# Performance work log

Hardware: AMD Instinct MI355X
Metric: run time of the kernel (lower is better)

The kernel has to match this reference:

```python
import jax, jax.numpy as jnp
import numpy as np

B, T, C, H = 2, 2048, 1024, 16
D = C // H  # head_dim = 64
CH = C // 2


def _ln(x, g, b, eps=1e-5):
    m = x.mean(-1, keepdims=True)
    v = ((x - m) ** 2).mean(-1, keepdims=True)
    return (x - m) / jnp.sqrt(v + eps) * g + b


def setup_inputs() -> dict:
    key = jax.random.key(0)
    ks = iter(jax.random.split(key, 32))
    w = lambda shp: jax.random.normal(next(ks), shp, dtype=jnp.float32) * 0.02
    inp = {
        'x': jax.random.normal(next(ks), (B, T, C), dtype=jnp.float32),
        'attention_mask': jnp.ones((B, T, T), dtype=jnp.int32),
        # importance_net: Linear(C,C/2), LN(C/2), GELU, Linear(C/2,1), Sigmoid
        'imp_w1': w((C, CH)), 'imp_b1': jnp.zeros((CH,)),
        'imp_g': jnp.ones((CH,)), 'imp_beta': jnp.zeros((CH,)),
        'imp_w2': w((CH, 1)), 'imp_b2': jnp.zeros((1,)),
        # reasoning_net: Linear(C,C), LN(C), GELU, Linear(C,C)
        'rsn_w1': w((C, C)), 'rsn_b1': jnp.zeros((C,)),
        'rsn_g': jnp.ones((C,)), 'rsn_beta': jnp.zeros((C,)),
        'rsn_w2': w((C, C)), 'rsn_b2': jnp.zeros((C,)),
        # attention projections
        'q_w': w((C, C)), 'q_b': jnp.zeros((C,)),
        'k_w': w((C, C)), 'k_b': jnp.zeros((C,)),
        'v_w': w((C, C)), 'v_b': jnp.zeros((C,)),
        'o_w': w((C, C)), 'o_b': jnp.zeros((C,)),
        # temp_net: Linear(C,C/2), LN(C/2), GELU, Linear(C/2,H)
        'tmp_w1': w((C, CH)), 'tmp_b1': jnp.zeros((CH,)),
        'tmp_g': jnp.ones((CH,)), 'tmp_beta': jnp.zeros((CH,)),
        'tmp_w2': w((CH, H)), 'tmp_b2': jnp.zeros((H,)),
        # output LayerNorm
        'norm_g': jnp.ones((C,)), 'norm_b': jnp.zeros((C,)),
    }
    return inp


def reference(x, attention_mask, imp_w1, imp_b1, imp_g, imp_beta, imp_w2, imp_b2,
              rsn_w1, rsn_b1, rsn_g, rsn_beta, rsn_w2, rsn_b2,
              q_w, q_b, k_w, k_b, v_w, v_b, o_w, o_b,
              tmp_w1, tmp_b1, tmp_g, tmp_beta, tmp_w2, tmp_b2,
              norm_g, norm_b):
    Bz, Tz, Cz = x.shape
    # importance gating: [B,T,1]
    h = jax.nn.gelu(_ln(x @ imp_w1 + imp_b1, imp_g, imp_beta), approximate=False)
    importance = jnp.maximum(jax.nn.sigmoid(h @ imp_w2 + imp_b2), 1e-6)
    xi = x * importance
    # reasoning net on gated input
    h = jax.nn.gelu(_ln(xi @ rsn_w1 + rsn_b1, rsn_g, rsn_beta), approximate=False)
    reasoned = h @ rsn_w2 + rsn_b2
    # projections
    q = (reasoned @ q_w + q_b).reshape(Bz, Tz, H, D).transpose(0, 2, 1, 3)
    k = (xi @ k_w + k_b).reshape(Bz, Tz, H, D).transpose(0, 2, 1, 3)
    v = (x @ v_w + v_b).reshape(Bz, Tz, H, D).transpose(0, 2, 1, 3)
    # per-(batch,head) temperature
    ht = jax.nn.gelu(_ln(reasoned.mean(axis=1) @ tmp_w1 + tmp_b1, tmp_g, tmp_beta), approximate=False)
    temp = jax.nn.softplus(ht @ tmp_w2 + tmp_b2) + 0.5  # [B,H]
    # attention with mask and learned temperature before softmax
    scale = 1.0 / jnp.sqrt(jnp.float32(D))
    attn = jnp.einsum('bhqd,bhkd->bhqk', q, k) * scale
    attn = jnp.where(attention_mask[:, None] == 0, -jnp.inf, attn)
    attn = attn * temp[:, :, None, None]
    attn = jax.nn.softmax(attn, axis=-1)
    # dropout is identity in eval mode
    out = jnp.einsum('bhqk,bhkd->bhqd', attn, v)
    out = out.transpose(0, 2, 1, 3).reshape(Bz, Tz, Cz)
    out = out @ o_w + o_b
    return _ln(x + out, norm_g, norm_b)
```

## Files before the change

kernel.cpp:

```cpp
#include <hip/hip_runtime.h>
#include <hip/hip_bf16.h>
#include <math.h>

#define BB 2
#define TT 2048
#define CC 1024
#define HH 16
#define DD 64
#define CHALF 512
#define NN (BB * TT)
#define LOG2E 1.44269504088896340736f

typedef __attribute__((ext_vector_type(8))) short short8;
typedef __attribute__((ext_vector_type(4))) short short4_t;
typedef __attribute__((ext_vector_type(4))) float f32x4;

__device__ __forceinline__ float gelu_exact(float x) {
    return 0.5f * x * (1.0f + erff(x * 0.70710678118654752f));
}

__device__ __forceinline__ short f2bf(float f) {
    __hip_bfloat16 h = __float2bfloat16(f);
    short s;
    __builtin_memcpy(&s, &h, 2);
    return s;
}

__device__ __forceinline__ void async_copy16(const void* g, void* l) {
    __builtin_amdgcn_global_load_lds(
        (const __attribute__((address_space(1))) void*)g,
        (__attribute__((address_space(3))) void*)l, 16, 0, 0);
}

__global__ __launch_bounds__(256) void prep(
    const float* __restrict__ x, __hip_bfloat16* __restrict__ x_bf,
    const int* __restrict__ mask, int* __restrict__ flags,
    const float* w0, const float* w1, const float* w2, const float* w3,
    const float* w4, const float* w5, const float* w6,
    __hip_bfloat16* t0, __hip_bfloat16* t1, __hip_bfloat16* t2,
    __hip_bfloat16* t3, __hip_bfloat16* t4, __hip_bfloat16* t5,
    __hip_bfloat16* t6) {
    __shared__ float T[64][65];
    int blk = blockIdx.x;
    int tid = threadIdx.x;
    if (blk < 2048) {
        int i = (blk * 256 + tid) * 8;
        float4 a = *(const float4*)&x[i];
        float4 b = *(const float4*)&x[i + 4];
        __hip_bfloat16 o[8] = {
            __float2bfloat16(a.x), __float2bfloat16(a.y),
            __float2bfloat16(a.z), __float2bfloat16(a.w),
            __float2bfloat16(b.x), __float2bfloat16(b.y),
            __float2bfloat16(b.z), __float2bfloat16(b.w)};
        *(float4*)&x_bf[i] = *(float4*)o;
    } else if (blk < 4096) {
        int idx = blk - 2048;
        int kt = idx & 31, qt = (idx >> 5) & 31, b = idx >> 10;
        int* red = (int*)T;
        int r = tid >> 2;
        int c0 = (tid & 3) * 16;
        const int* base =
            mask + ((size_t)(b * TT + qt * 64 + r)) * TT + kt * 64 + c0;
        int all = 1;
#pragma unroll
        for (int i = 0; i < 4; ++i) {
            int4 m4 = *(const int4*)(base + i * 4);
            all &= (m4.x != 0) & (m4.y != 0) & (m4.z != 0) & (m4.w != 0);
        }
        red[tid] = all;
        __syncthreads();
#pragma unroll
        for (int o = 128; o > 0; o >>= 1) {
            if (tid < o) red[tid] &= red[tid + o];
            __syncthreads();
        }
        if (tid == 0) flags[(b * 32 + qt) * 32 + kt] = red[0];
    } else {
        int idx = blk - 4096;
        const float* W;
        __hip_bfloat16* Wt;
        int N, n0, k0;
        if (idx < 128) {
            W = w0; Wt = t0; N = 512;
            n0 = (idx & 7) * 64;
            k0 = (idx >> 3) * 64;
        } else {
            idx -= 128;
            int w = idx >> 8;
            int r = idx & 255;
            N = 1024;
            n0 = (r & 15) * 64;
            k0 = (r >> 4) * 64;
            switch (w) {
                case 0: W = w1; Wt = t1; break;
                case 1: W = w2; Wt = t2; break;
                case 2: W = w3; Wt = t3; break;
                case 3: W = w4; Wt = t4; break;
                case 4: W = w5; Wt = t5; break;
                default: W = w6; Wt = t6; break;
            }
        }
        int c = tid & 63, r4 = tid >> 6;
#pragma unroll
        for (int i = 0; i < 16; ++i) {
            int row = i * 4 + r4;
            T[row][c] = W[(size_t)(k0 + row) * N + n0 + c];
        }
        __syncthreads();
#pragma unroll
        for (int i = 0; i < 16; ++i) {
            int row = i * 4 + r4;
            Wt[(size_t)(n0 + row) * CC + k0 + c] = __float2bfloat16(T[c][row]);
        }
    }
}

template <bool BF16OUT>
__global__ __launch_bounds__(256) void gemm_mfma64(
    const short* __restrict__ A, const short* __restrict__ Wt,
    const float* __restrict__ bias, float* __restrict__ Cf,
    __hip_bfloat16* __restrict__ Cb, int M, int N, int K) {
    __shared__ short As[64][32];
    __shared__ short Bs[128][32];
    int tid = threadIdx.x;
    int wave = tid >> 6, lane = tid & 63;
    int m16 = lane & 15, quad = lane >> 4;
    int wm = wave >> 1, wn = wave & 1;
    int row0 = blockIdx.y * 64, col0 = blockIdx.x * 128;
    int lr = lane >> 2;
    int kof = (lane & 3) * 8;

    f32x4 acc[2][4];
#pragma unroll
    for (int i = 0; i < 2; ++i)
#pragma unroll
        for (int j = 0; j < 4; ++j) acc[i][j] = (f32x4){0.f, 0.f, 0.f, 0.f};

    for (int k0 = 0; k0 < K; k0 += 32) {
        async_copy16(A + (size_t)(row0 + wave * 16 + lr) * K + k0 + kof,
                     &As[wave * 16][0]);
#pragma unroll
        for (int j = 0; j < 2; ++j) {
            int rbase = wave * 32 + j * 16;
            async_copy16(Wt + (size_t)(col0 + rbase + lr) * K + k0 + kof,
                         &Bs[rbase][0]);
        }
        __syncthreads();
        short8 af[2], bfr[4];
#pragma unroll
        for (int i = 0; i < 2; ++i)
            af[i] = *(const short8*)&As[wm * 32 + i * 16 + m16][quad * 8];
#pragma unroll
        for (int j = 0; j < 4; ++j)
            bfr[j] = *(const short8*)&Bs[wn * 64 + j * 16 + m16][quad * 8];
#pragma unroll
        for (int i = 0; i < 2; ++i)
#pragma unroll
            for (int j = 0; j < 4; ++j)
                acc[i][j] = __builtin_amdgcn_mfma_f32_16x16x32_bf16(
                    af[i], bfr[j], acc[i][j], 0, 0, 0);
        __syncthreads();
    }
#pragma unroll
    for (int i = 0; i < 2; ++i) {
#pragma unroll
        for (int j = 0; j < 4; ++j) {
            int col = col0 + wn * 64 + j * 16 + m16;
            float bv = bias[col];
#pragma unroll
            for (int rr = 0; rr < 4; ++rr) {
                int row = row0 + wm * 32 + i * 16 + quad * 4 + rr;
                float val = acc[i][j][rr] + bv;
                if (BF16OUT)
                    Cb[(size_t)row * N + col] = __float2bfloat16(val);
                else
                    Cf[(size_t)row * N + col] = val;
            }
        }
    }
}

__global__ __launch_bounds__(256) void gemm_qkv(
    const short* __restrict__ Aq, const short* __restrict__ Ak,
    const short* __restrict__ Av, const short* __restrict__ Wq,
    const short* __restrict__ Wk, const short* __restrict__ Wv,
    const float* __restrict__ bq, const float* __restrict__ bk,
    const float* __restrict__ bv, __hip_bfloat16* __restrict__ Cq,
    __hip_bfloat16* __restrict__ Ck, __hip_bfloat16* __restrict__ Cv,
    const float* __restrict__ tmp) {
    int z = blockIdx.z;
    const short* A = (z == 0) ? Aq : (z == 1) ? Ak : Av;
    const short* Wt = (z == 0) ? Wq : (z == 1) ? Wk : Wv;
    const float* bias = (z == 0) ? bq : (z == 1) ? bk : bv;
    __hip_bfloat16* C = (z == 0) ? Cq : (z == 1) ? Ck : Cv;

    __shared__ short As[128][32];
    __shared__ short Bs[128][32];
    int tid = threadIdx.x;
    int wave = tid >> 6, lane = tid & 63;
    int m16 = lane & 15, quad = lane >> 4;
    int wm = wave >> 1, wn = wave & 1;
    int row0 = blockIdx.y * 128, col0 = blockIdx.x * 128;
    int lr = lane >> 2;
    int kof = (lane & 3) * 8;

    float scale = 1.0f;
    if (z == 0)
        scale = tmp[(row0 >> 11) * HH + (col0 >> 6) + wn] * 0.125f * LOG2E;

    f32x4 acc[4][4];
#pragma unroll
    for (int i = 0; i < 4; ++i)
#pragma unroll
        for (int j = 0; j < 4; ++j) acc[i][j] = (f32x4){0.f, 0.f, 0.f, 0.f};

    for (int k0 = 0; k0 < CC; k0 += 32) {
#pragma unroll
        for (int j = 0; j < 2; ++j) {
            int rbase = wave * 32 + j * 16;
            async_copy16(A + (size_t)(row0 + rbase + lr) * CC + k0 + kof,
                         &As[rbase][0]);
            async_copy16(Wt + (size_t)(col0 + rbase + lr) * CC + k0 + kof,
                         &Bs[rbase][0]);
        }
        __syncthreads();
        short8 af[4], bfr[4];
#pragma unroll
        for (int i = 0; i < 4; ++i)
            af[i] = *(const short8*)&As[wm * 64 + i * 16 + m16][quad * 8];
#pragma unroll
        for (int j = 0; j < 4; ++j)
            bfr[j] = *(const short8*)&Bs[wn * 64 + j * 16 + m16][quad * 8];
#pragma unroll
        for (int i = 0; i < 4; ++i)
#pragma unroll
            for (int j = 0; j < 4; ++j)
                acc[i][j] = __builtin_amdgcn_mfma_f32_16x16x32_bf16(
                    af[i], bfr[j], acc[i][j], 0, 0, 0);
        __syncthreads();
    }
#pragma unroll
    for (int i = 0; i < 4; ++i) {
#pragma unroll
        for (int j = 0; j < 4; ++j) {
            int col = col0 + wn * 64 + j * 16 + m16;
            float bv2 = bias[col];
#pragma unroll
            for (int rr = 0; rr < 4; ++rr) {
                int row = row0 + wm * 64 + i * 16 + quad * 4 + rr;
                C[(size_t)row * CC + col] =
                    __float2bfloat16((acc[i][j][rr] + bv2) * scale);
            }
        }
    }
}

__global__ __launch_bounds__(256) void imp_fused(
    const float* __restrict__ h1, const float* __restrict__ g,
    const float* __restrict__ beta, const float* __restrict__ w2,
    const float* __restrict__ b2, const float* __restrict__ x,
    __hip_bfloat16* __restrict__ xi) {
    int row = blockIdx.x;
    int tid = threadIdx.x;
    const float* hr = h1 + (size_t)row * CHALF;
    float v0 = hr[tid], v1 = hr[tid + 256];
    __shared__ float red[256];
    red[tid] = v0 + v1;
    __syncthreads();
#pragma unroll
    for (int o = 128; o > 0; o >>= 1) {
        if (tid < o) red[tid] += red[tid + o];
        __syncthreads();
    }
    float mean = red[0] * (1.0f / CHALF);
    __syncthreads();
    float d0 = v0 - mean, d1 = v1 - mean;
    red[tid] = d0 * d0 + d1 * d1;
    __syncthreads();
#pragma unroll
    for (int o = 128; o > 0; o >>= 1) {
        if (tid < o) red[tid] += red[tid + o];
        __syncthreads();
    }
    float inv = rsqrtf(red[0] * (1.0f / CHALF) + 1e-5f);
    __syncthreads();
    float ge0 = gelu_exact(d0 * inv * g[tid] + beta[tid]);
    float ge1 = gelu_exact(d1 * inv * g[tid + 256] + beta[tid + 256]);
    red[tid] = ge0 * w2[tid] + ge1 * w2[tid + 256];
    __syncthreads();
#pragma unroll
    for (int o = 128; o > 0; o >>= 1) {
        if (tid < o) red[tid] += red[tid + o];
        __syncthreads();
    }
    float z = red[0] + b2[0];
    float sg = 1.0f / (1.0f + expf(-z));
    float imp = fmaxf(sg, 1e-6f);
#pragma unroll
    for (int i = 0; i < 4; ++i) {
        int c = i * 256 + tid;
        xi[(size_t)row * CC + c] =
            __float2bfloat16(x[(size_t)row * CC + c] * imp);
    }
}

template <int WIDTH>
__global__ __launch_bounds__(256) void ln_gelu_bf16(
    const float* __restrict__ Y, const float* __restrict__ g,
    const float* __restrict__ beta, __hip_bfloat16* __restrict__ O) {
    constexpr int PT = WIDTH / 256;
    int row = blockIdx.x;
    int tid = threadIdx.x;
    const float* yr = Y + (size_t)row * WIDTH;
    float v[PT];
    float s = 0.f;
#pragma unroll
    for (int i = 0; i < PT; ++i) {
        v[i] = yr[i * 256 + tid];
        s += v[i];
    }
    __shared__ float red[256];
    red[tid] = s;
    __syncthreads();
#pragma unroll
    for (int o = 128; o > 0; o >>= 1) {
        if (tid < o) red[tid] += red[tid + o];
        __syncthreads();
    }
    float mean = red[0] * (1.0f / WIDTH);
    __syncthreads();
    s = 0.f;
#pragma unroll
    for (int i = 0; i < PT; ++i) {
        float d = v[i] - mean;
        s += d * d;
    }
    red[tid] = s;
    __syncthreads();
#pragma unroll
    for (int o = 128; o > 0; o >>= 1) {
        if (tid < o) red[tid] += red[tid + o];
        __syncthreads();
    }
    float inv = rsqrtf(red[0] * (1.0f / WIDTH) + 1e-5f);
#pragma unroll
    for (int i = 0; i < PT; ++i) {
        int c = i * 256 + tid;
        O[(size_t)row * WIDTH + c] =
            __float2bfloat16(gelu_exact((v[i] - mean) * inv * g[c] + beta[c]));
    }
}

__global__ __launch_bounds__(256) void mean_part(
    const __hip_bfloat16* __restrict__ R, float* __restrict__ part) {
    int idx = blockIdx.x * 256 + threadIdx.x;
    int c = idx & (CC - 1);
    int chunk = (idx >> 10) & 15;
    int b = idx >> 14;
    const __hip_bfloat16* base = R + ((size_t)(b * TT + chunk * 128)) * CC + c;
    float s = 0.f;
    for (int t = 0; t < 128; ++t) s += __bfloat162float(base[(size_t)t * CC]);
    part[idx] = s;
}

__global__ __launch_bounds__(256) void temp_gemv1(
    const float* __restrict__ part, const float* __restrict__ w1,
    const float* __restrict__ b1, float* __restrict__ acc1) {
    __shared__ float rm_l[CC];
    __shared__ float red[256];
    int b = blockIdx.y;
    int c0 = blockIdx.x * 64;
    int tid = threadIdx.x;
    for (int cc = tid; cc < CC; cc += 256) {
        float s = 0.f;
#pragma unroll
        for (int ch = 0; ch < 16; ++ch)
            s += part[(size_t)(b * 16 + ch) * CC + cc];
        rm_l[cc] = s * (1.0f / TT);
    }
    __syncthreads();
    int col = c0 + (tid & 63);
    int kq = tid >> 6;
    float s = 0.f;
#pragma unroll 8
    for (int i = kq * 256; i < kq * 256 + 256; ++i)
        s = fmaf(rm_l[i], w1[(size_t)i * CHALF + col], s);
    red[tid] = s;
    __syncthreads();
    if (tid < 64) {
        float t = red[tid] + red[tid + 64] + red[tid + 128] + red[tid + 192];
        acc1[b * CHALF + tid + c0] = t + b1[col];
    }
}

__global__ __launch_bounds__(512) void temp_fin(
    const float* __restrict__ acc1, const float* __restrict__ g,
    const float* __restrict__ beta, const float* __restrict__ w2,
    const float* __restrict__ b2, float* __restrict__ temp) {
    __shared__ float red[512];
    __shared__ float wred[8][16];
    int b = blockIdx.x;
    int tid = threadIdx.x;
    int wave = tid >> 6, lane = tid & 63;
    float acc = acc1[b * CHALF + tid];
    red[tid] = acc;
    __syncthreads();
#pragma unroll
    for (int o = 256; o > 0; o >>= 1) {
        if (tid < o) red[tid] += red[tid + o];
        __syncthreads();
    }
    float mean = red[0] * (1.0f / CHALF);
    __syncthreads();
    float d = acc - mean;
    red[tid] = d * d;
    __syncthreads();
#pragma unroll
    for (int o = 256; o > 0; o >>= 1) {
        if (tid < o) red[tid] += red[tid + o];
        __syncthreads();
    }
    float inv = rsqrtf(red[0] * (1.0f / CHALF) + 1e-5f);
    float ht = gelu_exact((acc - mean) * inv * g[tid] + beta[tid]);
    float p[16];
#pragma unroll
    for (int j = 0; j < 16; ++j) p[j] = ht * w2[tid * HH + j];
#pragma unroll
    for (int off = 1; off < 64; off <<= 1)
#pragma unroll
        for (int j = 0; j < 16; ++j) p[j] += __shfl_xor(p[j], off, 64);
    if (lane == 0)
#pragma unroll
        for (int j = 0; j < 16; ++j) wred[wave][j] = p[j];
    __syncthreads();
    if (tid < HH) {
        float s = b2[tid];
#pragma unroll
        for (int w = 0; w < 8; ++w) s += wred[w][tid];
        float sp = fmaxf(s, 0.f) + log1pf(expf(-fabsf(s)));
        temp[b * HH + tid] = sp + 0.5f;
    }
}

__global__ __launch_bounds__(256) void transpose_v(
    const short* __restrict__ vb, short* __restrict__ vt) {
    __shared__ short T[64][72];
    int t0 = blockIdx.x * 64;
    int bh = blockIdx.y;
    int b = bh >> 4, h = bh & 15;
    int tid = threadIdx.x;
#pragma unroll
    for (int p = 0; p < 2; ++p) {
        int idx = p * 256 + tid;
        int r = idx >> 3, c = (idx & 7) * 8;
        *(short8*)&T[r][c] =
            *(const short8*)&vb[(size_t)(b * TT + t0 + r) * CC + h * DD + c];
    }
    __syncthreads();
#pragma unroll
    for (int p = 0; p < 2; ++p) {
        int idx = p * 256 + tid;
        int d = idx >> 3, c = (idx & 7) * 8;
        short8 o;
#pragma unroll
        for (int u = 0; u < 8; ++u) o[u] = T[c + u][d];
        *(short8*)&vt[((size_t)bh * DD + d) * TT + t0 + c] = o;
    }
}

__global__ __launch_bounds__(256) void flash_attn_mfma(
    const short* __restrict__ q, const short* __restrict__ k,
    const short* __restrict__ vt, const int* __restrict__ mask,
    const int* __restrict__ flags, __hip_bfloat16* __restrict__ out) {
    __shared__ short Ks[64][72];
    __shared__ short Vt[64][72];
    __shared__ short Ps[64][72];
    int tid = threadIdx.x;
    int wave = tid >> 6, lane = tid & 63;
    int m16 = lane & 15, quad = lane >> 4;
    int qt = blockIdx.x;
    int q0 = qt * 64;
    int bh = blockIdx.y;
    int b = bh >> 4, h = bh & 15;

    const short* qrow =
        q + ((size_t)(b * TT + q0 + wave * 16 + m16)) * CC + h * DD + quad * 8;
    short8 qf0 = *(const short8*)(qrow);
    short8 qf1 = *(const short8*)(qrow + 32);

    float m_run = -INFINITY, l_run = 0.f;
    f32x4 acc_o[4];
#pragma unroll
    for (int t = 0; t < 4; ++t) acc_o[t] = (f32x4){0.f, 0.f, 0.f, 0.f};

    for (int kt = 0; kt < TT / 64; ++kt) {
        int kb = kt * 64;
#pragma unroll
        for (int i = 0; i < 2; ++i) {
            int idx = i * 256 + tid;
            int r = idx >> 3;
            int dc = (idx & 7) * 8;
            *(short8*)&Ks[r][dc] =
                *(const short8*)(k + ((size_t)(b * TT + kb + r)) * CC + h * DD + dc);
            *(short8*)&Vt[r][dc] =
                *(const short8*)(vt + ((size_t)bh * DD + r) * TT + kb + dc);
        }
        __syncthreads();

        f32x4 sacc[4];
#pragma unroll
        for (int t = 0; t < 4; ++t) sacc[t] = (f32x4){0.f, 0.f, 0.f, 0.f};
#pragma unroll
        for (int t = 0; t < 4; ++t) {
            short8 kf0 = *(const short8*)&Ks[t * 16 + m16][quad * 8];
            sacc[t] = __builtin_amdgcn_mfma_f32_16x16x32_bf16(kf0, qf0, sacc[t], 0, 0, 0);
            short8 kf1 = *(const short8*)&Ks[t * 16 + m16][32 + quad * 8];
            sacc[t] = __builtin_amdgcn_mfma_f32_16x16x32_bf16(kf1, qf1, sacc[t], 0, 0, 0);
        }
        float sv[4][4];
#pragma unroll
        for (int t = 0; t < 4; ++t)
#pragma unroll
            for (int r = 0; r < 4; ++r) sv[t][r] = sacc[t][r];
        if (flags[(b * 32 + qt) * 32 + kt] == 0) {
            int qrg = q0 + wave * 16 + m16;
#pragma unroll
            for (int t = 0; t < 4; ++t)
#pragma unroll
                for (int r = 0; r < 4; ++r) {
                    int kg = kb + t * 16 + quad * 4 + r;
                    if (mask[((size_t)(b * TT + qrg)) * TT + kg] == 0)
                        sv[t][r] = -INFINITY;
                }
        }
        float mx = sv[0][0];
#pragma unroll
        for (int t = 0; t < 4; ++t)
#pragma unroll
            for (int r = 0; r < 4; ++r) mx = fmaxf(mx, sv[t][r]);
        mx = fmaxf(mx, __shfl_xor(mx, 16, 64));
        mx = fmaxf(mx, __shfl_xor(mx, 32, 64));
        float mnew = fmaxf(m_run, mx);
        float alpha = exp2f(m_run - mnew);
        m_run = mnew;
        int prow = wave * 16 + m16;
        float psum = 0.f;
#pragma unroll
        for (int t = 0; t < 4; ++t) {
            short4_t pk;
#pragma unroll
            for (int r = 0; r < 4; ++r) {
                float p = exp2f(sv[t][r] - mnew);
                psum += p;
                pk[r] = f2bf(p);
            }
            *(short4_t*)&Ps[prow][t * 16 + quad * 4] = pk;
        }
        psum += __shfl_xor(psum, 16, 64);
        psum += __shfl_xor(psum, 32, 64);
        l_run = l_run * alpha + psum;
#pragma unroll
        for (int r = 0; r < 4; ++r) {
            float ar = __shfl(alpha, (lane & 48) | (quad * 4 + r), 64);
#pragma unroll
            for (int td = 0; td < 4; ++td) acc_o[td][r] *= ar;
        }

#pragma unroll
        for (int kc = 0; kc < 2; ++kc) {
            short8 pf = *(const short8*)&Ps[wave * 16 + m16][kc * 32 + quad * 8];
#pragma unroll
            for (int td = 0; td < 4; ++td) {
                short8 vf = *(const short8*)&Vt[td * 16 + m16][kc * 32 + quad * 8];
                acc_o[td] = __builtin_amdgcn_mfma_f32_16x16x32_bf16(
                    pf, vf, acc_o[td], 0, 0, 0);
            }
        }
        __syncthreads();
    }

#pragma unroll
    for (int r = 0; r < 4; ++r) {
        float lr = __shfl(l_run, (lane & 48) | (quad * 4 + r), 64);
        float inv = 1.0f / lr;
        int row = b * TT + q0 + wave * 16 + quad * 4 + r;
#pragma unroll
        for (int td = 0; td < 4; ++td)
            out[(size_t)row * CC + h * DD + td * 16 + m16] =
                __float2bfloat16(acc_o[td][r] * inv);
    }
}

__global__ __launch_bounds__(256) void final_ln(
    const float* __restrict__ x, const float* __restrict__ p,
    const float* __restrict__ g, const float* __restrict__ beta,
    float* __restrict__ out) {
    int row = blockIdx.x;
    int tid = threadIdx.x;
    const float* xr = x + (size_t)row * CC;
    const float* pr = p + (size_t)row * CC;
    float v[4];
    float s = 0.f;
#pragma unroll
    for (int i = 0; i < 4; ++i) {
        int c = i * 256 + tid;
        v[i] = xr[c] + pr[c];
        s += v[i];
    }
    __shared__ float red[256];
    red[tid] = s;
    __syncthreads();
#pragma unroll
    for (int o = 128; o > 0; o >>= 1) {
        if (tid < o) red[tid] += red[tid + o];
        __syncthreads();
    }
    float mean = red[0] * (1.0f / CC);
    __syncthreads();
    s = 0.f;
#pragma unroll
    for (int i = 0; i < 4; ++i) {
        float d = v[i] - mean;
        s += d * d;
    }
    red[tid] = s;
    __syncthreads();
#pragma unroll
    for (int o = 128; o > 0; o >>= 1) {
        if (tid < o) red[tid] += red[tid + o];
        __syncthreads();
    }
    float inv = rsqrtf(red[0] * (1.0f / CC) + 1e-5f);
#pragma unroll
    for (int i = 0; i < 4; ++i) {
        int c = i * 256 + tid;
        out[(size_t)row * CC + c] = (v[i] - mean) * inv * g[c] + beta[c];
    }
}

extern "C" void kernel_launch(void* const* d_in, const int* in_sizes, int n_in,
                              void* d_out, int out_size, void* d_ws,
                              size_t ws_size, hipStream_t stream) {
    const float* x        = (const float*)d_in[0];
    const int*   mask     = (const int*)d_in[1];
    const float* imp_w1   = (const float*)d_in[2];
    const float* imp_b1   = (const float*)d_in[3];
    const float* imp_g    = (const float*)d_in[4];
    const float* imp_beta = (const float*)d_in[5];
    const float* imp_w2   = (const float*)d_in[6];
    const float* imp_b2   = (const float*)d_in[7];
    const float* rsn_w1   = (const float*)d_in[8];
    const float* rsn_b1   = (const float*)d_in[9];
    const float* rsn_g    = (const float*)d_in[10];
    const float* rsn_beta = (const float*)d_in[11];
    const float* rsn_w2   = (const float*)d_in[12];
    const float* rsn_b2   = (const float*)d_in[13];
    const float* q_w      = (const float*)d_in[14];
    const float* q_b      = (const float*)d_in[15];
    const float* k_w      = (const float*)d_in[16];
    const float* k_b      = (const float*)d_in[17];
    const float* v_w      = (const float*)d_in[18];
    const float* v_b      = (const float*)d_in[19];
    const float* o_w      = (const float*)d_in[20];
    const float* o_b      = (const float*)d_in[21];
    const float* tmp_w1   = (const float*)d_in[22];
    const float* tmp_b1   = (const float*)d_in[23];
    const float* tmp_g    = (const float*)d_in[24];
    const float* tmp_beta = (const float*)d_in[25];
    const float* tmp_w2   = (const float*)d_in[26];
    const float* tmp_b2   = (const float*)d_in[27];
    const float* norm_g   = (const float*)d_in[28];
    const float* norm_b   = (const float*)d_in[29];
    float* out = (float*)d_out;
    float* ws  = (float*)d_ws;

    float* h1  = ws;
    float* h2  = ws + 2097152;
    __hip_bfloat16* x_bf  = (__hip_bfloat16*)(ws + 6291456);
    __hip_bfloat16* xi_bf = (__hip_bfloat16*)(ws + 8388608);
    __hip_bfloat16* h2b   = (__hip_bfloat16*)(ws + 10485760);
    __hip_bfloat16* rs_bf = (__hip_bfloat16*)(ws + 12582912);
    __hip_bfloat16* qb    = (__hip_bfloat16*)(ws + 14680064);
    __hip_bfloat16* kb    = (__hip_bfloat16*)(ws + 16777216);
    __hip_bfloat16* vb    = (__hip_bfloat16*)(ws + 18874368);
    __hip_bfloat16* vtb   = (__hip_bfloat16*)(ws + 20971520);
    __hip_bfloat16* imp_w1t = (__hip_bfloat16*)(ws + 23068672);
    __hip_bfloat16* rsn_w1t = (__hip_bfloat16*)(ws + 23330816);
    __hip_bfloat16* rsn_w2t = (__hip_bfloat16*)(ws + 23855104);
    __hip_bfloat16* q_wt    = (__hip_bfloat16*)(ws + 24379392);
    __hip_bfloat16* k_wt    = (__hip_bfloat16*)(ws + 24903680);
    __hip_bfloat16* v_wt    = (__hip_bfloat16*)(ws + 25427968);
    __hip_bfloat16* o_wt    = (__hip_bfloat16*)(ws + 25952256);
    float* tmp  = ws + 26478592;
    float* part = ws + 26479104;
    int*   flg  = (int*)(ws + 26511872);
    float* acc1 = ws + 26513920;

    dim3 blk(256);
    prep<<<5760, blk, 0, stream>>>(
        x, x_bf, mask, flg,
        imp_w1, rsn_w1, rsn_w2, q_w, k_w, v_w, o_w,
        imp_w1t, rsn_w1t, rsn_w2t, q_wt, k_wt, v_wt, o_wt);

    gemm_mfma64<false><<<dim3(CHALF / 128, NN / 64), blk, 0, stream>>>(
        (const short*)x_bf, (const short*)imp_w1t, imp_b1, h1, nullptr, NN, CHALF, CC);
    imp_fused<<<NN, blk, 0, stream>>>(h1, imp_g, imp_beta, imp_w2, imp_b2, x, xi_bf);
    gemm_mfma64<false><<<dim3(CC / 128, NN / 64), blk, 0, stream>>>(
        (const short*)xi_bf, (const short*)rsn_w1t, rsn_b1, h2, nullptr, NN, CC, CC);
    ln_gelu_bf16<CC><<<NN, blk, 0, stream>>>(h2, rsn_g, rsn_beta, h2b);
    gemm_mfma64<true><<<dim3(CC / 128, NN / 64), blk, 0, stream>>>(
        (const short*)h2b, (const short*)rsn_w2t, rsn_b2, nullptr, rs_bf, NN, CC, CC);
    mean_part<<<128, blk, 0, stream>>>(rs_bf, part);
    temp_gemv1<<<dim3(CHALF / 64, BB), blk, 0, stream>>>(part, tmp_w1, tmp_b1, acc1);
    temp_fin<<<BB, dim3(512), 0, stream>>>(acc1, tmp_g, tmp_beta, tmp_w2, tmp_b2, tmp);
    gemm_qkv<<<dim3(CC / 128, NN / 128, 3), blk, 0, stream>>>(
        (const short*)rs_bf, (const short*)xi_bf, (const short*)x_bf,
        (const short*)q_wt, (const short*)k_wt, (const short*)v_wt,
        q_b, k_b, v_b, qb, kb, vb, tmp);
    transpose_v<<<dim3(TT / 64, BB * HH), blk, 0, stream>>>(
        (const short*)vb, (short*)vtb);
    flash_attn_mfma<<<dim3(TT / 64, BB * HH), blk, 0, stream>>>(
        (const short*)qb, (const short*)kb, (const short*)vtb, mask, flg, rs_bf);
    gemm_mfma64<false><<<dim3(CC / 128, NN / 64), blk, 0, stream>>>(
        (const short*)rs_bf, (const short*)o_wt, o_b, h2, nullptr, NN, CC, CC);
    final_ln<<<NN, blk, 0, stream>>>(x, h2, norm_g, norm_b, out);
}
```

Before: 443.2 us.

## Fuse V transpose into QKV GEMM epilogue and double flash-attention query tile

```diff
diff --git a/kernel.cpp b/kernel.cpp
--- a/kernel.cpp
+++ b/kernel.cpp
@@ -24,6 +24,17 @@
     short s;
     __builtin_memcpy(&s, &h, 2);
     return s;
+}
+
+__device__ __forceinline__ short4_t pack_bf16x4(float a, float b, float c,
+                                                float d) {
+    union {
+        __hip_bfloat162 h2[2];
+        short4_t s4;
+    } u;
+    u.h2[0] = __float22bfloat162_rn(make_float2(a, b));
+    u.h2[1] = __float22bfloat162_rn(make_float2(c, d));
+    return u.s4;
 }
 
 __device__ __forceinline__ void async_copy16(const void* g, void* l) {
@@ -192,7 +203,6 @@
     const short* A = (z == 0) ? Aq : (z == 1) ? Ak : Av;
     const short* Wt = (z == 0) ? Wq : (z == 1) ? Wk : Wv;
     const float* bias = (z == 0) ? bq : (z == 1) ? bk : bv;
-    __hip_bfloat16* C = (z == 0) ? Cq : (z == 1) ? Ck : Cv;
 
     __shared__ short As[128][32];
     __shared__ short Bs[128][32];
@@ -239,17 +249,37 @@
                     af[i], bfr[j], acc[i][j], 0, 0, 0);
         __syncthreads();
     }
-#pragma unroll
-    for (int i = 0; i < 4; ++i) {
-#pragma unroll
-        for (int j = 0; j < 4; ++j) {
-            int col = col0 + wn * 64 + j * 16 + m16;
-            float bv2 = bias[col];
-#pragma unroll
-            for (int rr = 0; rr < 4; ++rr) {
-                int row = row0 + wm * 64 + i * 16 + quad * 4 + rr;
-                C[(size_t)row * CC + col] =
-                    __float2bfloat16((acc[i][j][rr] + bv2) * scale);
+    if (z == 2) {
+        int b = row0 >> 11;
+        int t0r = (row0 & (TT - 1)) + wm * 64 + quad * 4;
+#pragma unroll
+        for (int i = 0; i < 4; ++i) {
+#pragma unroll
+            for (int j = 0; j < 4; ++j) {
+                int col = col0 + wn * 64 + j * 16 + m16;
+                int h = col >> 6, d = col & 63;
+                float bv2 = bias[col];
+                short4_t pk = pack_bf16x4(
+                    acc[i][j][0] + bv2, acc[i][j][1] + bv2,
+                    acc[i][j][2] + bv2, acc[i][j][3] + bv2);
+                *(short4_t*)&Cv[(((size_t)(b * HH + h) * DD) + d) * TT + t0r +
+                                i * 16] = pk;
+            }
+        }
+    } else {
+        __hip_bfloat16* C = (z == 0) ? Cq : Ck;
+#pragma unroll
+        for (int i = 0; i < 4; ++i) {
+#pragma unroll
+            for (int j = 0; j < 4; ++j) {
+                int col = col0 + wn * 64 + j * 16 + m16;
+                float bv2 = bias[col];
+#pragma unroll
+                for (int rr = 0; rr < 4; ++rr) {
+                    int row = row0 + wm * 64 + i * 16 + quad * 4 + rr;
+                    C[(size_t)row * CC + col] =
+                        __float2bfloat16((acc[i][j][rr] + bv2) * scale);
+                }
             }
         }
     }
@@ -442,56 +472,37 @@
     }
 }
 
-__global__ __launch_bounds__(256) void transpose_v(
-    const short* __restrict__ vb, short* __restrict__ vt) {
-    __shared__ short T[64][72];
-    int t0 = blockIdx.x * 64;
-    int bh = blockIdx.y;
-    int b = bh >> 4, h = bh & 15;
-    int tid = threadIdx.x;
-#pragma unroll
-    for (int p = 0; p < 2; ++p) {
-        int idx = p * 256 + tid;
-        int r = idx >> 3, c = (idx & 7) * 8;
-        *(short8*)&T[r][c] =
-            *(const short8*)&vb[(size_t)(b * TT + t0 + r) * CC + h * DD + c];
-    }
-    __syncthreads();
-#pragma unroll
-    for (int p = 0; p < 2; ++p) {
-        int idx = p * 256 + tid;
-        int d = idx >> 3, c = (idx & 7) * 8;
-        short8 o;
-#pragma unroll
-        for (int u = 0; u < 8; ++u) o[u] = T[c + u][d];
-        *(short8*)&vt[((size_t)bh * DD + d) * TT + t0 + c] = o;
-    }
-}
-
 __global__ __launch_bounds__(256) void flash_attn_mfma(
     const short* __restrict__ q, const short* __restrict__ k,
     const short* __restrict__ vt, const int* __restrict__ mask,
     const int* __restrict__ flags, __hip_bfloat16* __restrict__ out) {
     __shared__ short Ks[64][72];
     __shared__ short Vt[64][72];
-    __shared__ short Ps[64][72];
+    __shared__ short Ps[128][72];
     int tid = threadIdx.x;
     int wave = tid >> 6, lane = tid & 63;
     int m16 = lane & 15, quad = lane >> 4;
     int qt = blockIdx.x;
-    int q0 = qt * 64;
+    int q0 = qt * 128;
     int bh = blockIdx.y;
     int b = bh >> 4, h = bh & 15;
 
-    const short* qrow =
-        q + ((size_t)(b * TT + q0 + wave * 16 + m16)) * CC + h * DD + quad * 8;
-    short8 qf0 = *(const short8*)(qrow);
-    short8 qf1 = *(const short8*)(qrow + 32);
-
-    float m_run = -INFINITY, l_run = 0.f;
-    f32x4 acc_o[4];
-#pragma unroll
-    for (int t = 0; t < 4; ++t) acc_o[t] = (f32x4){0.f, 0.f, 0.f, 0.f};
+    short8 qf[2][2];
+#pragma unroll
+    for (int qg = 0; qg < 2; ++qg) {
+        const short* qrow = q + ((size_t)(b * TT + q0 + wave * 32 + qg * 16 + m16)) * CC +
+                            h * DD + quad * 8;
+        qf[qg][0] = *(const short8*)(qrow);
+        qf[qg][1] = *(const short8*)(qrow + 32);
+    }
+
+    float m_run[2] = {-INFINITY, -INFINITY};
+    float l_run[2] = {0.f, 0.f};
+    f32x4 acc_o[2][4];
+#pragma unroll
+    for (int qg = 0; qg < 2; ++qg)
+#pragma unroll
+        for (int t = 0; t < 4; ++t) acc_o[qg][t] = (f32x4){0.f, 0.f, 0.f, 0.f};
 
     for (int kt = 0; kt < TT / 64; ++kt) {
         int kb = kt * 64;
@@ -507,87 +518,103 @@
         }
         __syncthreads();
 
-        f32x4 sacc[4];
-#pragma unroll
-        for (int t = 0; t < 4; ++t) sacc[t] = (f32x4){0.f, 0.f, 0.f, 0.f};
+        short8 kf[4][2];
 #pragma unroll
         for (int t = 0; t < 4; ++t) {
-            short8 kf0 = *(const short8*)&Ks[t * 16 + m16][quad * 8];
-            sacc[t] = __builtin_amdgcn_mfma_f32_16x16x32_bf16(kf0, qf0, sacc[t], 0, 0, 0);
-            short8 kf1 = *(const short8*)&Ks[t * 16 + m16][32 + quad * 8];
-            sacc[t] = __builtin_amdgcn_mfma_f32_16x16x32_bf16(kf1, qf1, sacc[t], 0, 0, 0);
-        }
-        float sv[4][4];
-#pragma unroll
-        for (int t = 0; t < 4; ++t)
-#pragma unroll
-            for (int r = 0; r < 4; ++r) sv[t][r] = sacc[t][r];
-        if (flags[(b * 32 + qt) * 32 + kt] == 0) {
-            int qrg = q0 + wave * 16 + m16;
+            kf[t][0] = *(const short8*)&Ks[t * 16 + m16][quad * 8];
+            kf[t][1] = *(const short8*)&Ks[t * 16 + m16][32 + quad * 8];
+        }
+        int fl = flags[(b * 32 + 2 * qt + (wave >> 1)) * 32 + kt];
+
+#pragma unroll
+        for (int qg = 0; qg < 2; ++qg) {
+            f32x4 sacc[4];
+#pragma unroll
+            for (int t = 0; t < 4; ++t) sacc[t] = (f32x4){0.f, 0.f, 0.f, 0.f};
+#pragma unroll
+            for (int t = 0; t < 4; ++t) {
+                sacc[t] = __builtin_amdgcn_mfma_f32_16x16x32_bf16(kf[t][0], qf[qg][0], sacc[t], 0, 0, 0);
+                sacc[t] = __builtin_amdgcn_mfma_f32_16x16x32_bf16(kf[t][1], qf[qg][1], sacc[t], 0, 0, 0);
+            }
+            float sv[4][4];
 #pragma unroll
             for (int t = 0; t < 4; ++t)
 #pragma unroll
-                for (int r = 0; r < 4; ++r) {
-                    int kg = kb + t * 16 + quad * 4 + r;
-                    if (mask[((size_t)(b * TT + qrg)) * TT + kg] == 0)
-                        sv[t][r] = -INFINITY;
-                }
-        }
-        float mx = sv[0][0];
-#pragma unroll
-        for (int t = 0; t < 4; ++t)
-#pragma unroll
-            for (int r = 0; r < 4; ++r) mx = fmaxf(mx, sv[t][r]);
-        mx = fmaxf(mx, __shfl_xor(mx, 16, 64));
-        mx = fmaxf(mx, __shfl_xor(mx, 32, 64));
-        float mnew = fmaxf(m_run, mx);
-        float alpha = exp2f(m_run - mnew);
-        m_run = mnew;
-        int prow = wave * 16 + m16;
-        float psum = 0.f;
-#pragma unroll
-        for (int t = 0; t < 4; ++t) {
-            short4_t pk;
+                for (int r = 0; r < 4; ++r) sv[t][r] = sacc[t][r];
+            if (fl == 0) {
+                int qrow = q0 + wave * 32 + qg * 16 + m16;
+#pragma unroll
+                for (int t = 0; t < 4; ++t)
+#pragma unroll
+                    for (int r = 0; r < 4; ++r) {
+                        int kg = kb + t * 16 + quad * 4 + r;
+                        if (mask[((size_t)(b * TT + qrow)) * TT + kg] == 0)
+                            sv[t][r] = -INFINITY;
+                    }
+            }
+            float mx = sv[0][0];
+#pragma unroll
+            for (int t = 0; t < 4; ++t)
+#pragma unroll
+                for (int r = 0; r < 4; ++r) mx = fmaxf(mx, sv[t][r]);
+            mx = fmaxf(mx, __shfl_xor(mx, 16, 64));
+            mx = fmaxf(mx, __shfl_xor(mx, 32, 64));
+            float mnew = fmaxf(m_run[qg], mx);
+            float alpha = exp2f(m_run[qg] - mnew);
+            m_run[qg] = mnew;
+            int prow = wave * 32 + qg * 16 + m16;
+            float psum = 0.f;
+#pragma unroll
+            for (int t = 0; t < 4; ++t) {
+                float p0 = exp2f(sv[t][0] - mnew);
+                float p1 = exp2f(sv[t][1] - mnew);
+                float p2 = exp2f(sv[t][2] - mnew);
+                float p3 = exp2f(sv[t][3] - mnew);
+                psum += (p0 + p1) + (p2 + p3);
+                *(short4_t*)&Ps[prow][t * 16 + quad * 4] =
+                    pack_bf16x4(p0, p1, p2, p3);
+            }
+            psum += __shfl_xor(psum, 16, 64);
+            psum += __shfl_xor(psum, 32, 64);
+            l_run[qg] = l_run[qg] * alpha + psum;
 #pragma unroll
             for (int r = 0; r < 4; ++r) {
-                float p = exp2f(sv[t][r] - mnew);
-                psum += p;
-                pk[r] = f2bf(p);
-            }
-            *(short4_t*)&Ps[prow][t * 16 + quad * 4] = pk;
-        }
-        psum += __shfl_xor(psum, 16, 64);
-        psum += __shfl_xor(psum, 32, 64);
-        l_run = l_run * alpha + psum;
+                float ar = __shfl(alpha, (lane & 48) | (quad * 4 + r), 64);
+#pragma unroll
+                for (int td = 0; td < 4; ++td) acc_o[qg][td][r] *= ar;
+            }
+        }
+
+#pragma unroll
+        for (int kc = 0; kc < 2; ++kc) {
+            short8 vf[4];
+#pragma unroll
+            for (int td = 0; td < 4; ++td)
+                vf[td] = *(const short8*)&Vt[td * 16 + m16][kc * 32 + quad * 8];
+#pragma unroll
+            for (int qg = 0; qg < 2; ++qg) {
+                short8 pf = *(const short8*)&Ps[wave * 32 + qg * 16 + m16][kc * 32 + quad * 8];
+#pragma unroll
+                for (int td = 0; td < 4; ++td)
+                    acc_o[qg][td] = __builtin_amdgcn_mfma_f32_16x16x32_bf16(
+                        pf, vf[td], acc_o[qg][td], 0, 0, 0);
+            }
+        }
+        __syncthreads();
+    }
+
+#pragma unroll
+    for (int qg = 0; qg < 2; ++qg) {
 #pragma unroll
         for (int r = 0; r < 4; ++r) {
-            float ar = __shfl(alpha, (lane & 48) | (quad * 4 + r), 64);
-#pragma unroll
-            for (int td = 0; td < 4; ++td) acc_o[td][r] *= ar;
-        }
-
-#pragma unroll
-        for (int kc = 0; kc < 2; ++kc) {
-            short8 pf = *(const short8*)&Ps[wave * 16 + m16][kc * 32 + quad * 8];
-#pragma unroll
-            for (int td = 0; td < 4; ++td) {
-                short8 vf = *(const short8*)&Vt[td * 16 + m16][kc * 32 + quad * 8];
-                acc_o[td] = __builtin_amdgcn_mfma_f32_16x16x32_bf16(
-                    pf, vf, acc_o[td], 0, 0, 0);
-            }
-        }
-        __syncthreads();
-    }
-
-#pragma unroll
-    for (int r = 0; r < 4; ++r) {
-        float lr = __shfl(l_run, (lane & 48) | (quad * 4 + r), 64);
-        float inv = 1.0f / lr;
-        int row = b * TT + q0 + wave * 16 + quad * 4 + r;
-#pragma unroll
-        for (int td = 0; td < 4; ++td)
-            out[(size_t)row * CC + h * DD + td * 16 + m16] =
-                __float2bfloat16(acc_o[td][r] * inv);
+            float lr = __shfl(l_run[qg], (lane & 48) | (quad * 4 + r), 64);
+            float inv = 1.0f / lr;
+            int row = b * TT + q0 + wave * 32 + qg * 16 + quad * 4 + r;
+#pragma unroll
+            for (int td = 0; td < 4; ++td)
+                out[(size_t)row * CC + h * DD + td * 16 + m16] =
+                    __float2bfloat16(acc_o[qg][td][r] * inv);
+        }
     }
 }
 
@@ -682,7 +709,6 @@
     __hip_bfloat16* rs_bf = (__hip_bfloat16*)(ws + 12582912);
     __hip_bfloat16* qb    = (__hip_bfloat16*)(ws + 14680064);
     __hip_bfloat16* kb    = (__hip_bfloat16*)(ws + 16777216);
-    __hip_bfloat16* vb    = (__hip_bfloat16*)(ws + 18874368);
     __hip_bfloat16* vtb   = (__hip_bfloat16*)(ws + 20971520);
     __hip_bfloat16* imp_w1t = (__hip_bfloat16*)(ws + 23068672);
     __hip_bfloat16* rsn_w1t = (__hip_bfloat16*)(ws + 23330816);
@@ -716,10 +742,8 @@
     gemm_qkv<<<dim3(CC / 128, NN / 128, 3), blk, 0, stream>>>(
         (const short*)rs_bf, (const short*)xi_bf, (const short*)x_bf,
         (const short*)q_wt, (const short*)k_wt, (const short*)v_wt,
-        q_b, k_b, v_b, qb, kb, vb, tmp);
-    transpose_v<<<dim3(TT / 64, BB * HH), blk, 0, stream>>>(
-        (const short*)vb, (short*)vtb);
-    flash_attn_mfma<<<dim3(TT / 64, BB * HH), blk, 0, stream>>>(
+        q_b, k_b, v_b, qb, kb, vtb, tmp);
+    flash_attn_mfma<<<dim3(TT / 128, BB * HH), blk, 0, stream>>>(
         (const short*)qb, (const short*)kb, (const short*)vtb, mask, flg, rs_bf);
     gemm_mfma64<false><<<dim3(CC / 128, NN / 64), blk, 0, stream>>>(
         (const short*)rs_bf, (const short*)o_wt, o_b, h2, nullptr, NN, CC, CC);
```

New measurement: 441.7 us. Within noise of the previous version (-0.3%).
